# Optimization experiments

Hardware: AMD Instinct MI355X
Metric: run time of the kernel (lower is better)

## Reference

```python
import jax, jax.numpy as jnp
import numpy as np

B, S, HID, NH = 2, 2048, 2048, 16
HD = HID // NH          # head_size = 128
ROPE_THETA = 10000.0
SCALING = HD ** -0.5


def setup_inputs() -> dict:
    key = jax.random.key(0)
    ks = jax.random.split(key, 8)
    std = 1.0 / np.sqrt(HID)
    inp = {
        "hidden_states": jax.random.normal(ks[0], (B, S, HID), jnp.float32),
        "positions": jnp.broadcast_to(jnp.arange(S, dtype=jnp.int32), (B, S)),
        "wq": jax.random.normal(ks[1], (HID, HID), jnp.float32) * std,
        "bq": jax.random.normal(ks[2], (HID,), jnp.float32) * 0.02,
        "wk": jax.random.normal(ks[3], (HID, HID), jnp.float32) * std,
        "bk": jax.random.normal(ks[4], (HID,), jnp.float32) * 0.02,
        "wv": jax.random.normal(ks[5], (HID, HID), jnp.float32) * std,
        "bv": jax.random.normal(ks[6], (HID,), jnp.float32) * 0.02,
        "wc": jax.random.normal(ks[7], (HID, HID), jnp.float32) * std,
    }
    return inp


def _rope_neox(x, positions):
    # x: [B, S, NH, HD]; positions: [B, S] int
    half = HD // 2
    inv_freq = 1.0 / (ROPE_THETA ** (jnp.arange(half, dtype=jnp.float32) * (2.0 / HD)))
    freqs = positions.astype(jnp.float32)[..., None] * inv_freq      # [B,S,half]
    cos = jnp.cos(freqs)[:, :, None, :]                               # [B,S,1,half]
    sin = jnp.sin(freqs)[:, :, None, :]
    x1, x2 = x[..., :half], x[..., half:]
    return jnp.concatenate([x1 * cos - x2 * sin, x2 * cos + x1 * sin], axis=-1)


def reference(hidden_states, positions, wq, bq, wk, bk, wv, bv, wc):
    # fused QKV projections
    q = hidden_states @ wq + bq
    k = hidden_states @ wk + bk
    v = hidden_states @ wv + bv
    q = q.reshape(B, S, NH, HD)
    k = k.reshape(B, S, NH, HD)
    v = v.reshape(B, S, NH, HD)
    # neox-style rotary embedding over full head dim
    q = _rope_neox(q, positions)
    k = _rope_neox(k, positions)
    # causal self-attention (prefill path of RadixAttention)
    scores = jnp.einsum("bqhd,bkhd->bhqk", q, k) * SCALING
    causal = jnp.tril(jnp.ones((S, S), dtype=bool))
    scores = jnp.where(causal, scores, jnp.finfo(scores.dtype).min)
    probs = jax.nn.softmax(scores, axis=-1)
    attn = jnp.einsum("bhqk,bkhd->bqhd", probs, v).reshape(B, S, HID)
    # output projection (no bias)
    return attn @ wc
```

## Files before the change

kernel.cpp:

```cpp
#include <hip/hip_runtime.h>
#include <stdint.h>

constexpr int Bsz = 2;
constexpr int Ssz = 2048;
constexpr int Hid = 2048;
constexpr int NHd = 16;
constexpr int Hd  = 128;
constexpr int Mrows = Bsz * Ssz;

typedef __bf16 bf16;
typedef __bf16 bf16x8 __attribute__((ext_vector_type(8)));
typedef __bf16 bf16x4 __attribute__((ext_vector_type(4)));
typedef float  f32x4  __attribute__((ext_vector_type(4)));
typedef float  f32x16 __attribute__((ext_vector_type(16)));

__device__ __forceinline__ void gload_lds16(const bf16* g, bf16* l) {
  __builtin_amdgcn_global_load_lds((const __attribute__((address_space(1))) void*)g,
                                   (__attribute__((address_space(3))) void*)l, 16, 0, 0);
}

__device__ __forceinline__ uint32_t pkbf(bf16 a, bf16 b) {
  union { bf16 hh[2]; uint32_t u; } x;
  x.hh[0] = a; x.hh[1] = b;
  return x.u;
}
__device__ __forceinline__ uint32_t pkff(float a, float b) {
  return pkbf((bf16)a, (bf16)b);
}

__global__ void k_cvt(const float* __restrict__ in, bf16* __restrict__ out, int n4) {
  int i = blockIdx.x * blockDim.x + threadIdx.x;
  if (i >= n4) return;
  float4 v = ((const float4*)in)[i];
  bf16x4 o = { (bf16)v.x, (bf16)v.y, (bf16)v.z, (bf16)v.w };
  ((bf16x4*)out)[i] = o;
}

__global__ void k_wtrans(const float* __restrict__ w0, const float* __restrict__ w1,
                         const float* __restrict__ w2, const float* __restrict__ w3,
                         bf16* __restrict__ out) {
  __shared__ float tile[32][33];
  int z = blockIdx.z;
  const float* w = (z == 0) ? w0 : (z == 1) ? w1 : (z == 2) ? w2 : w3;
  bf16* o = out + (size_t)z * Hid * Hid;
  int n0 = blockIdx.x * 32, k0 = blockIdx.y * 32;
  int tx = threadIdx.x, ty = threadIdx.y;
#pragma unroll
  for (int i = 0; i < 4; i++)
    tile[ty + i * 8][tx] = w[(size_t)(k0 + ty + i * 8) * Hid + n0 + tx];
  __syncthreads();
#pragma unroll
  for (int i = 0; i < 4; i++)
    o[(size_t)(n0 + ty + i * 8) * Hid + k0 + tx] = (bf16)tile[tx][ty + i * 8];
}

__device__ __forceinline__ bf16x8 rdfrag(const bf16* t, int row, int kslot) {
  return *(const bf16x8*)((const char*)t + row * 128 + (((kslot ^ (row & 7)) & 7) << 4));
}

__device__ __forceinline__ void stage_half(const bf16* g, bf16* l, int w, int lane) {
  const int rsub = lane >> 3;
  const int slot = (lane & 7) ^ rsub;
#pragma unroll
  for (int j = 0; j < 2; ++j) {
    const int blk = w * 2 + j;
    gload_lds16(g + (size_t)(blk * 8 + rsub) * Hid + slot * 8, l + blk * 512);
  }
}

__device__ __forceinline__ void stage_192(const bf16* g, bf16* l, int w, int lane) {
  const int rsub = lane >> 3;
  const int slot = (lane & 7) ^ rsub;
#pragma unroll
  for (int j = 0; j < 3; ++j) {
    const int blk = w * 3 + j;
    gload_lds16(g + (size_t)(blk * 8 + rsub) * Hid + slot * 8, l + blk * 512);
  }
}

#define PH_SYNC()                                      \
  __builtin_amdgcn_s_barrier();                        \
  asm volatile("s_waitcnt lgkmcnt(0)" ::: "memory");   \
  __builtin_amdgcn_sched_barrier(0);

__global__ __launch_bounds__(512, 1) void k_qkv(const bf16* __restrict__ A,
                                                const bf16* __restrict__ Bt,
                                                const float* __restrict__ biasq,
                                                const float* __restrict__ biask,
                                                const float* __restrict__ biasv,
                                                bf16* __restrict__ Qo, bf16* __restrict__ Ko,
                                                bf16* __restrict__ Vo) {
  constexpr int KK = Hid;
  constexpr int NT = KK / 64;
  __shared__ bf16 smA[2][256 * 64];
  __shared__ bf16 smB[2][192 * 64];
  const int hw = blockIdx.y * gridDim.x + blockIdx.x;
  const int chunk = hw & 7, within = hw >> 3;
  const int cr = chunk & 1, cc = chunk >> 1;
  const int mt = cr * 8 + (within & 7);
  const int nt = cc * 8 + (within >> 3);
  const int m0 = mt * 256, n0 = nt * 192;
  const int tid = threadIdx.x, lane = tid & 63, w = tid >> 6;
  const int wm = w >> 2, wn = w & 3;
  const int frow = lane & 15, a4 = lane >> 4;
  const bf16* Ag = A + (size_t)m0 * KK;
  const bf16* Bg = Bt + (size_t)n0 * KK;
  f32x4 acc[8][3] = {};
  stage_half(Ag,                    smA[0],            w, lane);
  stage_half(Ag + (size_t)128 * KK, smA[0] + 128 * 64, w, lane);
  stage_192 (Bg,                    smB[0],            w, lane);
  asm volatile("s_waitcnt vmcnt(0)" ::: "memory");
  __builtin_amdgcn_s_barrier();
  for (int kt = 0; kt < NT; ++kt) {
    const bf16* At  = smA[kt & 1];
    const bf16* Btl = smB[kt & 1];
    bf16* As2 = smA[(kt + 1) & 1];
    bf16* Bs2 = smB[(kt + 1) & 1];
    const bool more = (kt + 1) < NT;
    const size_t kn = (size_t)(kt + 1) * 64;
    bf16x8 afA[4][2], afB[4][2], bfr[3][2];
#pragma unroll
    for (int f = 0; f < 4; ++f)
#pragma unroll
      for (int kk = 0; kk < 2; ++kk)
        afA[f][kk] = rdfrag(At, wm * 128 + f * 16 + frow, kk * 4 + a4);
#pragma unroll
    for (int nf = 0; nf < 3; ++nf)
#pragma unroll
      for (int kk = 0; kk < 2; ++kk)
        bfr[nf][kk] = rdfrag(Btl, wn * 48 + nf * 16 + frow, kk * 4 + a4);
    if (more) {
      stage_half(Ag + kn,                    As2,            w, lane);
      stage_half(Ag + (size_t)128 * KK + kn, As2 + 128 * 64, w, lane);
    }
    PH_SYNC();
    __builtin_amdgcn_s_setprio(1);
#pragma unroll
    for (int f = 0; f < 4; ++f)
#pragma unroll
      for (int nf = 0; nf < 2; ++nf)
#pragma unroll
        for (int kk = 0; kk < 2; ++kk)
          acc[f][nf] = __builtin_amdgcn_mfma_f32_16x16x32_bf16(
              afA[f][kk], bfr[nf][kk], acc[f][nf], 0, 0, 0);
    __builtin_amdgcn_s_setprio(0);
    __builtin_amdgcn_s_barrier();
#pragma unroll
    for (int f = 0; f < 4; ++f)
#pragma unroll
      for (int kk = 0; kk < 2; ++kk)
        afB[f][kk] = rdfrag(At, wm * 128 + 64 + f * 16 + frow, kk * 4 + a4);
    if (more) stage_192(Bg + kn, Bs2, w, lane);
    PH_SYNC();
    __builtin_amdgcn_s_setprio(1);
#pragma unroll
    for (int f = 0; f < 4; ++f)
#pragma unroll
      for (int nf = 0; nf < 2; ++nf)
#pragma unroll
        for (int kk = 0; kk < 2; ++kk)
          acc[4 + f][nf] = __builtin_amdgcn_mfma_f32_16x16x32_bf16(
              afB[f][kk], bfr[nf][kk], acc[4 + f][nf], 0, 0, 0);
    __builtin_amdgcn_s_setprio(0);
    __builtin_amdgcn_s_barrier();
    __builtin_amdgcn_s_setprio(1);
#pragma unroll
    for (int f = 0; f < 4; ++f)
#pragma unroll
      for (int kk = 0; kk < 2; ++kk)
        acc[f][2] = __builtin_amdgcn_mfma_f32_16x16x32_bf16(
            afA[f][kk], bfr[2][kk], acc[f][2], 0, 0, 0);
#pragma unroll
    for (int f = 0; f < 4; ++f)
#pragma unroll
      for (int kk = 0; kk < 2; ++kk)
        acc[4 + f][2] = __builtin_amdgcn_mfma_f32_16x16x32_bf16(
            afB[f][kk], bfr[2][kk], acc[4 + f][2], 0, 0, 0);
    __builtin_amdgcn_s_setprio(0);
    asm volatile("s_waitcnt vmcnt(0)" ::: "memory");
    __builtin_amdgcn_sched_barrier(0);
    __builtin_amdgcn_s_barrier();
  }
#pragma unroll
  for (int nf = 0; nf < 3; ++nf) {
    const int col = n0 + wn * 48 + nf * 16 + frow;
    const int z = col >> 11;
    const float* bias = (z == 0) ? biasq : (z == 1) ? biask : biasv;
    bf16* o = (z == 0) ? Qo : (z == 1) ? Ko : Vo;
    const float oscale = (z == 1) ? (float)(0.08838834764831845 * 1.4426950408889634) : 1.0f;
    const float bb_ = bias[col & 2047];
    const int h = (col >> 7) & 15, hd = col & (Hd - 1);
#pragma unroll
    for (int mf = 0; mf < 8; ++mf) {
#pragma unroll
      for (int r = 0; r < 4; ++r) {
        const int row = m0 + wm * 128 + mf * 16 + a4 * 4 + r;
        const int bb = row >> 11, ss = row & (Ssz - 1);
        o[(((size_t)bb * NHd + h) * Ssz + ss) * Hd + hd] = (bf16)((acc[mf][nf][r] + bb_) * oscale);
      }
    }
  }
}

template <int CHM, int CHN>
__global__ __launch_bounds__(512, 1) void k_gemm(const bf16* __restrict__ A,
                                                 const bf16* __restrict__ Bt,
                                                 float* __restrict__ Fo) {
  constexpr int KK = Hid;
  constexpr int NT = KK / 64;
  __shared__ bf16 smA[2][256 * 64];
  __shared__ bf16 smB[2][128 * 64];
  const int hw = blockIdx.y * gridDim.x + blockIdx.x;
  const int chunk = hw & 7, within = hw >> 3;
  const int chunk_rows = gridDim.y / CHM;
  const int cr = chunk % chunk_rows, cc = chunk / chunk_rows;
  const int mt = cr * CHM + within % CHM;
  const int nt = cc * CHN + within / CHM;
  const int m0 = mt * 256, n0 = nt * 128;
  const int tid = threadIdx.x, lane = tid & 63, w = tid >> 6;
  const int wm = w >> 2, wn = w & 3;
  const int frow = lane & 15, a4 = lane >> 4;
  const bf16* Ag = A + (size_t)m0 * KK;
  const bf16* Bg = Bt + (size_t)n0 * KK;
  f32x4 acc[8][2] = {};
  stage_half(Ag,                    smA[0],            w, lane);
  stage_half(Ag + (size_t)128 * KK, smA[0] + 128 * 64, w, lane);
  stage_half(Bg,                    smB[0],            w, lane);
  stage_half(Bg + 64,               smB[1],            w, lane);
  asm volatile("s_waitcnt vmcnt(2)" ::: "memory");
  __builtin_amdgcn_sched_barrier(0);
  __builtin_amdgcn_s_barrier();
  for (int it = 0; it < NT / 2; ++it) {
    const int base = 2 * it;
    const bool has2 = (base + 2) < NT;
    const bool has3 = (base + 3) < NT;
    bf16x8 af[4][2], bfr[2][2];
#pragma unroll
    for (int f = 0; f < 4; ++f)
#pragma unroll
      for (int kk = 0; kk < 2; ++kk)
        af[f][kk] = rdfrag(smA[0], wm * 128 + f * 16 + frow, kk * 4 + a4);
#pragma unroll
    for (int nf = 0; nf < 2; ++nf)
#pragma unroll
      for (int kk = 0; kk < 2; ++kk)
        bfr[nf][kk] = rdfrag(smB[0], wn * 32 + nf * 16 + frow, kk * 4 + a4);
    {
      const size_t kA1 = (size_t)(base + 1) * 64;
      stage_half(Ag + kA1,                    smA[1],            w, lane);
      stage_half(Ag + (size_t)128 * KK + kA1, smA[1] + 128 * 64, w, lane);
    }
    PH_SYNC();
    __builtin_amdgcn_s_setprio(1);
#pragma unroll
    for (int f = 0; f < 4; ++f)
#pragma unroll
      for (int nf = 0; nf < 2; ++nf)
#pragma unroll
        for (int kk = 0; kk < 2; ++kk)
          acc[f][nf] = __builtin_amdgcn_mfma_f32_16x16x32_bf16(
              af[f][kk], bfr[nf][kk], acc[f][nf], 0, 0, 0);
    __builtin_amdgcn_s_setprio(0);
    __builtin_amdgcn_s_barrier();
#pragma unroll
    for (int f = 0; f < 4; ++f)
#pragma unroll
      for (int kk = 0; kk < 2; ++kk)
        af[f][kk] = rdfrag(smA[0], wm * 128 + (4 + f) * 16 + frow, kk * 4 + a4);
    if (has2) stage_half(Bg + (size_t)(base + 2) * 64, smB[0], w, lane);
    PH_SYNC();
    __builtin_amdgcn_s_setprio(1);
#pragma unroll
    for (int f = 0; f < 4; ++f)
#pragma unroll
      for (int nf = 0; nf < 2; ++nf)
#pragma unroll
        for (int kk = 0; kk < 2; ++kk)
          acc[4 + f][nf] = __builtin_amdgcn_mfma_f32_16x16x32_bf16(
              af[f][kk], bfr[nf][kk], acc[4 + f][nf], 0, 0, 0);
    __builtin_amdgcn_s_setprio(0);
    if (has2) { asm volatile("s_waitcnt vmcnt(2)" ::: "memory"); }
    else      { asm volatile("s_waitcnt vmcnt(0)" ::: "memory"); }
    __builtin_amdgcn_sched_barrier(0);
    __builtin_amdgcn_s_barrier();
#pragma unroll
    for (int f = 0; f < 4; ++f)
#pragma unroll
      for (int kk = 0; kk < 2; ++kk)
        af[f][kk] = rdfrag(smA[1], wm * 128 + f * 16 + frow, kk * 4 + a4);
#pragma unroll
    for (int nf = 0; nf < 2; ++nf)
#pragma unroll
      for (int kk = 0; kk < 2; ++kk)
        bfr[nf][kk] = rdfrag(smB[1], wn * 32 + nf * 16 + frow, kk * 4 + a4);
    if (has2) {
      const size_t kA2 = (size_t)(base + 2) * 64;
      stage_half(Ag + kA2,                    smA[0],            w, lane);
      stage_half(Ag + (size_t)128 * KK + kA2, smA[0] + 128 * 64, w, lane);
    }
    PH_SYNC();
    __builtin_amdgcn_s_setprio(1);
#pragma unroll
    for (int f = 0; f < 4; ++f)
#pragma unroll
      for (int nf = 0; nf < 2; ++nf)
#pragma unroll
        for (int kk = 0; kk < 2; ++kk)
          acc[f][nf] = __builtin_amdgcn_mfma_f32_16x16x32_bf16(
              af[f][kk], bfr[nf][kk], acc[f][nf], 0, 0, 0);
    __builtin_amdgcn_s_setprio(0);
    __builtin_amdgcn_s_barrier();
#pragma unroll
    for (int f = 0; f < 4; ++f)
#pragma unroll
      for (int kk = 0; kk < 2; ++kk)
        af[f][kk] = rdfrag(smA[1], wm * 128 + (4 + f) * 16 + frow, kk * 4 + a4);
    if (has3) stage_half(Bg + (size_t)(base + 3) * 64, smB[1], w, lane);
    PH_SYNC();
    __builtin_amdgcn_s_setprio(1);
#pragma unroll
    for (int f = 0; f < 4; ++f)
#pragma unroll
      for (int nf = 0; nf < 2; ++nf)
#pragma unroll
        for (int kk = 0; kk < 2; ++kk)
          acc[4 + f][nf] = __builtin_amdgcn_mfma_f32_16x16x32_bf16(
              af[f][kk], bfr[nf][kk], acc[4 + f][nf], 0, 0, 0);
    __builtin_amdgcn_s_setprio(0);
    if (has2) {
      if (has3) { asm volatile("s_waitcnt vmcnt(2)" ::: "memory"); }
      else      { asm volatile("s_waitcnt vmcnt(0)" ::: "memory"); }
      __builtin_amdgcn_sched_barrier(0);
    }
    __builtin_amdgcn_s_barrier();
  }
#pragma unroll
  for (int mf = 0; mf < 8; ++mf)
#pragma unroll
    for (int nf = 0; nf < 2; ++nf) {
      const int col = n0 + wn * 32 + nf * 16 + frow;
#pragma unroll
      for (int r = 0; r < 4; ++r) {
        const int row = m0 + wm * 128 + mf * 16 + a4 * 4 + r;
        Fo[(size_t)row * Hid + col] = acc[mf][nf][r];
      }
    }
}

__global__ void k_rope(bf16* __restrict__ Q, bf16* __restrict__ Kk, const int* __restrict__ pos) {
  const int idx = blockIdx.x * 256 + threadIdx.x;
  const int i = idx & 63;
  const int s = (idx >> 6) & (Ssz - 1);
  const int bh = idx >> 17;
  const int b = bh >> 4;
  const float p = (float)pos[b * Ssz + s];
  const float f = p * exp2f(-(float)i * 0.20762050593046014f);
  float sn, cs;
  sincosf(f, &sn, &cs);
  const size_t base = ((size_t)bh * Ssz + s) * Hd;
  float x1 = (float)Q[base + i], x2 = (float)Q[base + i + 64];
  Q[base + i]      = (bf16)(x1 * cs - x2 * sn);
  Q[base + i + 64] = (bf16)(x2 * cs + x1 * sn);
  x1 = (float)Kk[base + i]; x2 = (float)Kk[base + i + 64];
  Kk[base + i]      = (bf16)(x1 * cs - x2 * sn);
  Kk[base + i + 64] = (bf16)(x2 * cs + x1 * sn);
}

__global__ __launch_bounds__(256, 2) void k_attn(const bf16* __restrict__ Qg,
                                                 const bf16* __restrict__ Kg,
                                                 const bf16* __restrict__ Vg,
                                                 bf16* __restrict__ AO) {
  const int bid = blockIdx.x;
  const int slot = bid & 255;
  const int bh = slot & 31;
  const int xch = slot >> 5;
  const int qc = (bid >> 8) ? (15 - xch) : xch;
  const int tid = threadIdx.x, lane = tid & 63, w = tid >> 6;
  const int l31 = lane & 31, h = lane >> 5;
  __shared__ bf16 Ks[2][64 * 128];
  __shared__ bf16 Vt[2][128 * 72];
  const size_t hbase = (size_t)bh * Ssz * Hd;
  const int q0 = qc * 128 + w * 32;
  bf16x8 qf[8];
  {
    const bf16* qp = Qg + hbase + (size_t)(q0 + l31) * Hd + h * 8;
#pragma unroll
    for (int c = 0; c < 8; c++) qf[c] = *(const bf16x8*)(qp + c * 16);
  }
  float m = -1e30f, lsum = 0.f;
  f32x16 o[4] = {};
  const int NT = 2 * (qc + 1);
  const int r4  = (tid >> 4) << 2;
  const int hd0 = (tid & 15) << 3;
  bf16x8 vv[4];
#pragma unroll
  for (int p = 0; p < 4; p++)
    vv[p] = *(const bf16x8*)(Vg + hbase + (size_t)(r4 + p) * Hd + hd0);
  __builtin_amdgcn_sched_barrier(0);
#pragma unroll
  for (int i = 0; i < 4; i++) {
    const int db  = (w * 4 + i) * 1024 + (lane << 4);
    const int row = db >> 8;
    const int cb  = (db & 255) ^ ((row & 7) << 4);
    gload_lds16(Kg + hbase + row * Hd + (cb >> 1), Ks[0] + (w * 4 + i) * 512);
  }
  for (int t = 0; t < NT; ++t) {
    const int kv0 = t * 64;
    const int cur = t & 1;
    asm volatile("s_waitcnt vmcnt(4)" ::: "memory");
#pragma unroll
    for (int j = 0; j < 8; j++) {
      uint2 wv;
      wv.x = pkbf(vv[0][j], vv[1][j]);
      wv.y = pkbf(vv[2][j], vv[3][j]);
      const int hd = hd0 + j;
      const int cb = (r4 * 2) ^ (((hd >> 3) & 7) << 4);
      *(uint2*)((char*)(Vt[cur]) + hd * 144 + cb) = wv;
    }
    const int tn = (t + 1 < NT) ? t + 1 : t;
    const size_t nb = (size_t)tn * 64;
#pragma unroll
    for (int p = 0; p < 4; p++)
      vv[p] = *(const bf16x8*)(Vg + hbase + (nb + r4 + p) * Hd + hd0);
    __builtin_amdgcn_sched_barrier(0);
#pragma unroll
    for (int i = 0; i < 4; i++) {
      const int db  = (w * 4 + i) * 1024 + (lane << 4);
      const int row = db >> 8;
      const int cb  = (db & 255) ^ ((row & 7) << 4);
      gload_lds16(Kg + hbase + (nb + row) * Hd + (cb >> 1), Ks[cur ^ 1] + (w * 4 + i) * 512);
    }
    asm volatile("s_waitcnt vmcnt(8) lgkmcnt(0)" ::: "memory");
    __builtin_amdgcn_sched_barrier(0);
    __builtin_amdgcn_s_barrier();
    if (kv0 <= q0 + 31) {
      const bf16* KsC = Ks[cur];
      const bf16* VtC = Vt[cur];
      f32x16 s0 = {}, s1 = {};
      __builtin_amdgcn_s_setprio(1);
#pragma unroll
      for (int c = 0; c < 8; c++) {
        const int cb = (c * 32 + h * 16) ^ ((l31 & 7) << 4);
        bf16x8 k0 = *(const bf16x8*)((const char*)KsC + l31 * 256 + cb);
        bf16x8 k1 = *(const bf16x8*)((const char*)KsC + (32 + l31) * 256 + cb);
        s0 = __builtin_amdgcn_mfma_f32_32x32x16_bf16(k0, qf[c], s0, 0, 0, 0);
        s1 = __builtin_amdgcn_mfma_f32_32x32x16_bf16(k1, qf[c], s1, 0, 0, 0);
      }
      __builtin_amdgcn_s_setprio(0);
      if (kv0 + 63 > q0) {
        const int qg = q0 + l31;
        const int kb = kv0 + 4 * h;
#pragma unroll
        for (int r = 0; r < 16; r++) {
          const int cr = (r & 3) + 8 * (r >> 2);
          if (kb + cr > qg)      s0[r] = -1e30f;
          if (kb + 32 + cr > qg) s1[r] = -1e30f;
        }
      }
      float tm = s0[0];
#pragma unroll
      for (int r = 1; r < 16; r++) tm = fmaxf(tm, s0[r]);
#pragma unroll
      for (int r = 0; r < 16; r++) tm = fmaxf(tm, s1[r]);
      tm = fmaxf(tm, __shfl_xor(tm, 32));
      if (!__all(tm - m <= 8.0f)) {
        const float mn = fmaxf(m, tm);
        const float rs = exp2f(m - mn);
        m = mn; lsum *= rs;
#pragma unroll
        for (int ct = 0; ct < 4; ct++)
#pragma unroll
          for (int r = 0; r < 16; r++) o[ct][r] *= rs;
      }
      float ps = 0.f;
#pragma unroll
      for (int r = 0; r < 16; r++) { s0[r] = exp2f(s0[r] - m); ps += s0[r]; }
#pragma unroll
      for (int r = 0; r < 16; r++) { s1[r] = exp2f(s1[r] - m); ps += s1[r]; }
      ps += __shfl_xor(ps, 32);
      lsum += ps;
      uint32_t gw[8][2];
#pragma unroll
      for (int g = 0; g < 4; g++) {
        gw[g][0]     = pkff(s0[4 * g], s0[4 * g + 1]);
        gw[g][1]     = pkff(s0[4 * g + 2], s0[4 * g + 3]);
        gw[4 + g][0] = pkff(s1[4 * g], s1[4 * g + 1]);
        gw[4 + g][1] = pkff(s1[4 * g + 2], s1[4 * g + 3]);
      }
#pragma unroll
      for (int kc = 0; kc < 4; kc++) {
        const uint32_t a0 = gw[2 * kc][0], a1 = gw[2 * kc][1];
        const uint32_t b0 = gw[2 * kc + 1][0], b1 = gw[2 * kc + 1][1];
        const uint32_t sd0 = h ? a0 : b0, sd1 = h ? a1 : b1;
        const uint32_t r0 = (uint32_t)__shfl_xor((int)sd0, 32);
        const uint32_t r1 = (uint32_t)__shfl_xor((int)sd1, 32);
        union { uint32_t u[4]; bf16x8 v; } pa;
        pa.u[0] = h ? r0 : a0; pa.u[1] = h ? r1 : a1;
        pa.u[2] = h ? b0 : r0; pa.u[3] = h ? b1 : r1;
        __builtin_amdgcn_s_setprio(1);
#pragma unroll
        for (int ct = 0; ct < 4; ct++) {
          const int row = ct * 32 + l31;
          const int cb = (kc * 32 + h * 16) ^ (((row >> 3) & 7) << 4);
          bf16x8 vf = *(const bf16x8*)((const char*)VtC + row * 144 + cb);
          o[ct] = __builtin_amdgcn_mfma_f32_32x32x16_bf16(pa.v, vf, o[ct], 0, 0, 0);
        }
        __builtin_amdgcn_s_setprio(0);
      }
    }
    __builtin_amdgcn_s_barrier();
  }
  const float linv = 1.0f / lsum;
  float li[16];
#pragma unroll
  for (int r = 0; r < 16; r++)
    li[r] = __shfl(linv, (r & 3) + 8 * (r >> 2) + 4 * h);
  const int b = bh >> 4, hh = bh & 15;
#pragma unroll
  for (int ct = 0; ct < 4; ct++) {
#pragma unroll
    for (int r = 0; r < 16; r++) {
      const int qrow = q0 + (r & 3) + 8 * (r >> 2) + 4 * h;
      AO[((size_t)b * Ssz + qrow) * Hid + hh * Hd + ct * 32 + l31] = (bf16)(o[ct][r] * li[r]);
    }
  }
}

extern "C" void kernel_launch(void* const* d_in, const int* in_sizes, int n_in,
                              void* d_out, int out_size, void* d_ws, size_t ws_size,
                              hipStream_t stream) {
  (void)in_sizes; (void)n_in; (void)out_size; (void)ws_size;
  const float* hidden   = (const float*)d_in[0];
  const int*   positions= (const int*)d_in[1];
  const float* wq = (const float*)d_in[2];
  const float* bq = (const float*)d_in[3];
  const float* wk = (const float*)d_in[4];
  const float* bk = (const float*)d_in[5];
  const float* wv = (const float*)d_in[6];
  const float* bv = (const float*)d_in[7];
  const float* wc = (const float*)d_in[8];
  float* out = (float*)d_out;

  char* ws = (char*)d_ws;
  bf16* WT  = (bf16*)ws;
  bf16* Hbf = (bf16*)(ws + (size_t)4 * Hid * Hid * 2);
  bf16* Qb  = (bf16*)(ws + (size_t)4 * Hid * Hid * 2 + (size_t)Mrows * Hid * 2);
  bf16* Kb  = Qb + (size_t)Mrows * Hid;
  bf16* Vb  = Kb + (size_t)Mrows * Hid;

  k_cvt<<<dim3(Mrows * Hid / 4 / 256), dim3(256), 0, stream>>>(hidden, Hbf, Mrows * Hid / 4);
  k_wtrans<<<dim3(Hid / 32, Hid / 32, 4), dim3(32, 8), 0, stream>>>(wq, wk, wv, wc, WT);
  k_qkv<<<dim3(32, 16), dim3(512), 0, stream>>>(
      Hbf, WT, bq, bk, bv, Qb, Kb, Vb);
  k_rope<<<dim3(Bsz * NHd * Ssz * 64 / 256), dim3(256), 0, stream>>>(Qb, Kb, positions);
  k_attn<<<dim3(512), dim3(256), 0, stream>>>(Qb, Kb, Vb, Hbf );
  k_gemm<8, 4><<<dim3(16, 16), dim3(512), 0, stream>>>(
      Hbf, WT + (size_t)3 * Hid * Hid, out);
}
```

Measured before the change: 261.4 us.

## Triple-buffer B tiles in GEMMs and vectorize weight transpose

Measured after the change: 261.6 us. About the same (+0.1%).

```diff
diff --git a/kernel.cpp b/kernel.cpp
--- a/kernel.cpp
+++ b/kernel.cpp
@@ -39,19 +39,33 @@
 __global__ void k_wtrans(const float* __restrict__ w0, const float* __restrict__ w1,
                          const float* __restrict__ w2, const float* __restrict__ w3,
                          bf16* __restrict__ out) {
-  __shared__ float tile[32][33];
-  int z = blockIdx.z;
+  __shared__ float tile[64][65];
+  const int z = blockIdx.z;
   const float* w = (z == 0) ? w0 : (z == 1) ? w1 : (z == 2) ? w2 : w3;
   bf16* o = out + (size_t)z * Hid * Hid;
-  int n0 = blockIdx.x * 32, k0 = blockIdx.y * 32;
-  int tx = threadIdx.x, ty = threadIdx.y;
-#pragma unroll
-  for (int i = 0; i < 4; i++)
-    tile[ty + i * 8][tx] = w[(size_t)(k0 + ty + i * 8) * Hid + n0 + tx];
+  const int n0 = blockIdx.x * 64, k0 = blockIdx.y * 64;
+  const int tid = threadIdx.x;
+  {
+    const int row = tid >> 4, col = (tid & 15) * 4;
+#pragma unroll
+    for (int i = 0; i < 4; i++) {
+      float4 v = *(const float4*)&w[(size_t)(k0 + row + i * 16) * Hid + n0 + col];
+      tile[row + i * 16][col + 0] = v.x;
+      tile[row + i * 16][col + 1] = v.y;
+      tile[row + i * 16][col + 2] = v.z;
+      tile[row + i * 16][col + 3] = v.w;
+    }
+  }
   __syncthreads();
-#pragma unroll
-  for (int i = 0; i < 4; i++)
-    o[(size_t)(n0 + ty + i * 8) * Hid + k0 + tx] = (bf16)tile[tx][ty + i * 8];
+  {
+    const int n = tid >> 2, ks = (tid & 3) * 16;
+    union { bf16x8 v[2]; bf16 e[16]; } pk;
+#pragma unroll
+    for (int j = 0; j < 16; j++) pk.e[j] = (bf16)tile[ks + j][n];
+    bf16* op = &o[(size_t)(n0 + n) * Hid + k0 + ks];
+    *(bf16x8*)op = pk.v[0];
+    *(bf16x8*)(op + 8) = pk.v[1];
+  }
 }
 
 __device__ __forceinline__ bf16x8 rdfrag(const bf16* t, int row, int kslot) {
@@ -93,7 +107,7 @@
   constexpr int KK = Hid;
   constexpr int NT = KK / 64;
   __shared__ bf16 smA[2][256 * 64];
-  __shared__ bf16 smB[2][192 * 64];
+  __shared__ bf16 smB[3][192 * 64];
   const int hw = blockIdx.y * gridDim.x + blockIdx.x;
   const int chunk = hw & 7, within = hw >> 3;
   const int cr = chunk & 1, cc = chunk >> 1;
@@ -109,15 +123,15 @@
   stage_half(Ag,                    smA[0],            w, lane);
   stage_half(Ag + (size_t)128 * KK, smA[0] + 128 * 64, w, lane);
   stage_192 (Bg,                    smB[0],            w, lane);
-  asm volatile("s_waitcnt vmcnt(0)" ::: "memory");
+  stage_192 (Bg + 64,               smB[1],            w, lane);
+  asm volatile("s_waitcnt vmcnt(3)" ::: "memory");
+  __builtin_amdgcn_sched_barrier(0);
   __builtin_amdgcn_s_barrier();
   for (int kt = 0; kt < NT; ++kt) {
     const bf16* At  = smA[kt & 1];
-    const bf16* Btl = smB[kt & 1];
-    bf16* As2 = smA[(kt + 1) & 1];
-    bf16* Bs2 = smB[(kt + 1) & 1];
-    const bool more = (kt + 1) < NT;
-    const size_t kn = (size_t)(kt + 1) * 64;
+    const bf16* Btl = smB[kt % 3];
+    const bool more1 = (kt + 1) < NT;
+    const bool more2 = (kt + 2) < NT;
     bf16x8 afA[4][2], afB[4][2], bfr[3][2];
 #pragma unroll
     for (int f = 0; f < 4; ++f)
@@ -129,7 +143,9 @@
 #pragma unroll
       for (int kk = 0; kk < 2; ++kk)
         bfr[nf][kk] = rdfrag(Btl, wn * 48 + nf * 16 + frow, kk * 4 + a4);
-    if (more) {
+    if (more1) {
+      bf16* As2 = smA[(kt + 1) & 1];
+      const size_t kn = (size_t)(kt + 1) * 64;
       stage_half(Ag + kn,                    As2,            w, lane);
       stage_half(Ag + (size_t)128 * KK + kn, As2 + 128 * 64, w, lane);
     }
@@ -150,7 +166,7 @@
 #pragma unroll
       for (int kk = 0; kk < 2; ++kk)
         afB[f][kk] = rdfrag(At, wm * 128 + 64 + f * 16 + frow, kk * 4 + a4);
-    if (more) stage_192(Bg + kn, Bs2, w, lane);
+    if (more2) stage_192(Bg + (size_t)(kt + 2) * 64, smB[(kt + 2) % 3], w, lane);
     PH_SYNC();
     __builtin_amdgcn_s_setprio(1);
 #pragma unroll
@@ -177,8 +193,11 @@
         acc[4 + f][2] = __builtin_amdgcn_mfma_f32_16x16x32_bf16(
             afB[f][kk], bfr[2][kk], acc[4 + f][2], 0, 0, 0);
     __builtin_amdgcn_s_setprio(0);
-    asm volatile("s_waitcnt vmcnt(0)" ::: "memory");
-    __builtin_amdgcn_sched_barrier(0);
+    if (more1) {
+      if (more2) { asm volatile("s_waitcnt vmcnt(3)" ::: "memory"); }
+      else       { asm volatile("s_waitcnt vmcnt(0)" ::: "memory"); }
+      __builtin_amdgcn_sched_barrier(0);
+    }
     __builtin_amdgcn_s_barrier();
   }
 #pragma unroll
@@ -209,7 +228,7 @@
   constexpr int KK = Hid;
   constexpr int NT = KK / 64;
   __shared__ bf16 smA[2][256 * 64];
-  __shared__ bf16 smB[2][128 * 64];
+  __shared__ bf16 smB[3][128 * 64];
   const int hw = blockIdx.y * gridDim.x + blockIdx.x;
   const int chunk = hw & 7, within = hw >> 3;
   const int chunk_rows = gridDim.y / CHM;
@@ -230,25 +249,27 @@
   asm volatile("s_waitcnt vmcnt(2)" ::: "memory");
   __builtin_amdgcn_sched_barrier(0);
   __builtin_amdgcn_s_barrier();
-  for (int it = 0; it < NT / 2; ++it) {
-    const int base = 2 * it;
-    const bool has2 = (base + 2) < NT;
-    const bool has3 = (base + 3) < NT;
-    bf16x8 af[4][2], bfr[2][2];
-#pragma unroll
-    for (int f = 0; f < 4; ++f)
-#pragma unroll
-      for (int kk = 0; kk < 2; ++kk)
-        af[f][kk] = rdfrag(smA[0], wm * 128 + f * 16 + frow, kk * 4 + a4);
+  for (int kt = 0; kt < NT; ++kt) {
+    const bf16* At  = smA[kt & 1];
+    const bf16* Btl = smB[kt % 3];
+    const bool more1 = (kt + 1) < NT;
+    const bool more2 = (kt + 2) < NT;
+    bf16x8 afA[4][2], afB[4][2], bfr[2][2];
+#pragma unroll
+    for (int f = 0; f < 4; ++f)
+#pragma unroll
+      for (int kk = 0; kk < 2; ++kk)
+        afA[f][kk] = rdfrag(At, wm * 128 + f * 16 + frow, kk * 4 + a4);
 #pragma unroll
     for (int nf = 0; nf < 2; ++nf)
 #pragma unroll
       for (int kk = 0; kk < 2; ++kk)
-        bfr[nf][kk] = rdfrag(smB[0], wn * 32 + nf * 16 + frow, kk * 4 + a4);
-    {
-      const size_t kA1 = (size_t)(base + 1) * 64;
-      stage_half(Ag + kA1,                    smA[1],            w, lane);
-      stage_half(Ag + (size_t)128 * KK + kA1, smA[1] + 128 * 64, w, lane);
+        bfr[nf][kk] = rdfrag(Btl, wn * 32 + nf * 16 + frow, kk * 4 + a4);
+    if (more1) {
+      bf16* As2 = smA[(kt + 1) & 1];
+      const size_t kn = (size_t)(kt + 1) * 64;
+      stage_half(Ag + kn,                    As2,            w, lane);
+      stage_half(Ag + (size_t)128 * KK + kn, As2 + 128 * 64, w, lane);
     }
     PH_SYNC();
     __builtin_amdgcn_s_setprio(1);
@@ -259,15 +280,15 @@
 #pragma unroll
         for (int kk = 0; kk < 2; ++kk)
           acc[f][nf] = __builtin_amdgcn_mfma_f32_16x16x32_bf16(
-              af[f][kk], bfr[nf][kk], acc[f][nf], 0, 0, 0);
+              afA[f][kk], bfr[nf][kk], acc[f][nf], 0, 0, 0);
     __builtin_amdgcn_s_setprio(0);
     __builtin_amdgcn_s_barrier();
 #pragma unroll
     for (int f = 0; f < 4; ++f)
 #pragma unroll
       for (int kk = 0; kk < 2; ++kk)
-        af[f][kk] = rdfrag(smA[0], wm * 128 + (4 + f) * 16 + frow, kk * 4 + a4);
-    if (has2) stage_half(Bg + (size_t)(base + 2) * 64, smB[0], w, lane);
+        afB[f][kk] = rdfrag(At, wm * 128 + 64 + f * 16 + frow, kk * 4 + a4);
+    if (more2) stage_half(Bg + (size_t)(kt + 2) * 64, smB[(kt + 2) % 3], w, lane);
     PH_SYNC();
     __builtin_amdgcn_s_setprio(1);
 #pragma unroll
@@ -277,59 +298,11 @@
 #pragma unroll
         for (int kk = 0; kk < 2; ++kk)
           acc[4 + f][nf] = __builtin_amdgcn_mfma_f32_16x16x32_bf16(
-              af[f][kk], bfr[nf][kk], acc[4 + f][nf], 0, 0, 0);
+              afB[f][kk], bfr[nf][kk], acc[4 + f][nf], 0, 0, 0);
     __builtin_amdgcn_s_setprio(0);
-    if (has2) { asm volatile("s_waitcnt vmcnt(2)" ::: "memory"); }
-    else      { asm volatile("s_waitcnt vmcnt(0)" ::: "memory"); }
-    __builtin_amdgcn_sched_barrier(0);
-    __builtin_amdgcn_s_barrier();
-#pragma unroll
-    for (int f = 0; f < 4; ++f)
-#pragma unroll
-      for (int kk = 0; kk < 2; ++kk)
-        af[f][kk] = rdfrag(smA[1], wm * 128 + f * 16 + frow, kk * 4 + a4);
-#pragma unroll
-    for (int nf = 0; nf < 2; ++nf)
-#pragma unroll
-      for (int kk = 0; kk < 2; ++kk)
-        bfr[nf][kk] = rdfrag(smB[1], wn * 32 + nf * 16 + frow, kk * 4 + a4);
-    if (has2) {
-      const size_t kA2 = (size_t)(base + 2) * 64;
-      stage_half(Ag + kA2,                    smA[0],            w, lane);
-      stage_half(Ag + (size_t)128 * KK + kA2, smA[0] + 128 * 64, w, lane);
-    }
-    PH_SYNC();
-    __builtin_amdgcn_s_setprio(1);
-#pragma unroll
-    for (int f = 0; f < 4; ++f)
-#pragma unroll
-      for (int nf = 0; nf < 2; ++nf)
-#pragma unroll
-        for (int kk = 0; kk < 2; ++kk)
-          acc[f][nf] = __builtin_amdgcn_mfma_f32_16x16x32_bf16(
-              af[f][kk], bfr[nf][kk], acc[f][nf], 0, 0, 0);
-    __builtin_amdgcn_s_setprio(0);
-    __builtin_amdgcn_s_barrier();
-#pragma unroll
-    for (int f = 0; f < 4; ++f)
-#pragma unroll
-      for (int kk = 0; kk < 2; ++kk)
-        af[f][kk] = rdfrag(smA[1], wm * 128 + (4 + f) * 16 + frow, kk * 4 + a4);
-    if (has3) stage_half(Bg + (size_t)(base + 3) * 64, smB[1], w, lane);
-    PH_SYNC();
-    __builtin_amdgcn_s_setprio(1);
-#pragma unroll
-    for (int f = 0; f < 4; ++f)
-#pragma unroll
-      for (int nf = 0; nf < 2; ++nf)
-#pragma unroll
-        for (int kk = 0; kk < 2; ++kk)
-          acc[4 + f][nf] = __builtin_amdgcn_mfma_f32_16x16x32_bf16(
-              af[f][kk], bfr[nf][kk], acc[4 + f][nf], 0, 0, 0);
-    __builtin_amdgcn_s_setprio(0);
-    if (has2) {
-      if (has3) { asm volatile("s_waitcnt vmcnt(2)" ::: "memory"); }
-      else      { asm volatile("s_waitcnt vmcnt(0)" ::: "memory"); }
+    if (more1) {
+      if (more2) { asm volatile("s_waitcnt vmcnt(2)" ::: "memory"); }
+      else       { asm volatile("s_waitcnt vmcnt(0)" ::: "memory"); }
       __builtin_amdgcn_sched_barrier(0);
     }
     __builtin_amdgcn_s_barrier();
@@ -549,7 +522,7 @@
   bf16* Vb  = Kb + (size_t)Mrows * Hid;
 
   k_cvt<<<dim3(Mrows * Hid / 4 / 256), dim3(256), 0, stream>>>(hidden, Hbf, Mrows * Hid / 4);
-  k_wtrans<<<dim3(Hid / 32, Hid / 32, 4), dim3(32, 8), 0, stream>>>(wq, wk, wv, wc, WT);
+  k_wtrans<<<dim3(Hid / 64, Hid / 64, 4), dim3(256), 0, stream>>>(wq, wk, wv, wc, WT);
   k_qkv<<<dim3(32, 16), dim3(512), 0, stream>>>(
       Hbf, WT, bq, bk, bv, Qb, Kb, Vb);
   k_rope<<<dim3(Bsz * NHd * Ssz * 64 / 256), dim3(256), 0, stream>>>(Qb, Kb, positions);
```
